# Performance work log

Measured on AMD Instinct MI355X. Metric: run time of the kernel, lower is better.

## Reference

```python
import jax, jax.numpy as jnp
import numpy as np

B, H, W, C = 8, 64, 64, 64


def setup_inputs() -> dict:
    key = jax.random.key(0)
    ks = jax.random.split(key, 9)
    s = 1.0 / np.sqrt(C)
    return {
        "x": jax.random.normal(ks[0], (B, H, W, C), dtype=jnp.float32),
        "wq": jax.random.uniform(ks[1], (C, C), jnp.float32, -s, s),
        "bq": jax.random.uniform(ks[2], (C,), jnp.float32, -s, s),
        "wk": jax.random.uniform(ks[3], (C, C), jnp.float32, -s, s),
        "bk": jax.random.uniform(ks[4], (C,), jnp.float32, -s, s),
        "wv": jax.random.uniform(ks[5], (C, C), jnp.float32, -s, s),
        "bv": jax.random.uniform(ks[6], (C,), jnp.float32, -s, s),
        "wp": jax.random.uniform(ks[7], (C, C), jnp.float32, -s, s),
        "bp": jax.random.uniform(ks[8], (C,), jnp.float32, -s, s),
    }


def reference(x, wq, bq, wk, bk, wv, bv, wp, bp):
    b, h, w, c = x.shape
    n = h * w
    xf = x.reshape(b, n, c)
    scale = c ** (-0.5)
    q = xf @ wq.T + bq  # [B,N,C]
    k = xf @ wk.T + bk
    v = xf @ wv.T + bv
    center_idx = (h // 2) * w + (w // 2)
    central = q[:, center_idx, :][:, None, :]           # [B,1,C]
    qb = jnp.broadcast_to(central, (b, n, c))           # rank-1 broadcast query
    pos = jnp.arange(n)
    dist = jnp.sqrt(((pos // w - h // 2) ** 2 + (pos % w - w // 2) ** 2).astype(jnp.float32))
    weights = jnp.exp(1.0 - dist)                       # [N]
    qw = qb * weights[None, :, None]
    attn = jnp.einsum('bnc,bmc->bnm', qw, k) * scale    # dense [B,N,N] (memory-bound)
    attn = jax.nn.softmax(attn, axis=-1)
    out = jnp.einsum('bnm,bmc->bnc', attn, v)
    out = out @ wp.T + bp
    return out.reshape(b, h, w, c)
```

## Files before the change

### kernel.cpp

```cpp
#include <hip/hip_runtime.h>

#define BB 8
#define NN 4096
#define CC 64
#define CENTER (32*64 + 32)
#define GTILE 16
#define MS 32
#define MSL (NN/MS)
#define CUT 64

struct Geom {
    short gid[2049];
    short g2d2[64];
    int ng;
};

constexpr Geom makeGeom() {
    Geom t{};
    bool occ[2049] = {};
    for (int y = 0; y < 64; ++y)
        for (int x = 0; x < 64; ++x) {
            int dy = y - 32, dx = x - 32;
            occ[dy*dy + dx*dx] = true;
        }
    int g = 0;
    for (int i = 0; i < CUT; ++i) {
        if (occ[i]) { t.gid[i] = (short)g; t.g2d2[g] = (short)i; ++g; }
        else t.gid[i] = (short)-1;
    }
    t.ng = g;
    for (int i = CUT; i <= 2048; ++i) t.gid[i] = occ[i] ? (short)g : (short)-1;
    return t;
}

constexpr int NGN = makeGeom().ng;
constexpr int NT  = (NGN + 1 + GTILE - 1) / GTILE;
constexpr int GE  = NT * GTILE;
static_assert(NGN + 1 <= GE, "group padding");
static_assert(MS * 8 == 256, "blockIdx decode shift");
__constant__ Geom GEOM = makeGeom();

constexpr int CST_WVPT = 0;
constexpr int CST_BVP  = 4096;
constexpr int CST_U    = 4160;
constexpr int CST_T    = 4672;
constexpr int CST_SIZE = 4736;

constexpr int OFF_CST  = 0;
constexpr int OFF_S    = CST_SIZE;
constexpr int OFF_VP   = OFF_S + BB*NN;
constexpr int OFF_PART = OFF_VP + BB*NN*CC;
constexpr int OFF_ZP   = OFF_PART + BB*MS*GE*CC;
constexpr int OFF_OG   = OFF_ZP + BB*MS*GE;

__global__ __launch_bounds__(256) void k_prep(
    const float* __restrict__ x,
    const float* __restrict__ wq, const float* __restrict__ bq,
    const float* __restrict__ wk, const float* __restrict__ bk,
    const float* __restrict__ wv, const float* __restrict__ bv,
    const float* __restrict__ wp,
    float* __restrict__ cst)
{
    const int tid = threadIdx.x;
    const int blk = blockIdx.x;
    if (blk < 8) {
        __shared__ float q_s[CC];
        const int b = blk;
        if (tid < CC) {
            const float* xc = x + ((size_t)b*NN + CENTER)*CC;
            float a = bq[tid];
            for (int i = 0; i < CC; ++i) a += xc[i] * wq[tid*CC + i];
            q_s[tid] = a;
        }
        __syncthreads();
        if (tid < CC) {
            float a = 0.f;
            for (int c = 0; c < CC; ++c) a += q_s[c] * wk[c*CC + tid];
            cst[CST_U + b*CC + tid] = a;
        }
        if (tid == 64) {
            float a = 0.f;
            for (int c = 0; c < CC; ++c) a += q_s[c] * bk[c];
            cst[CST_T + b] = a;
        }
    } else if (blk < 24) {
        const int idx = (blk - 8)*256 + tid;
        const int i = idx >> 6, c = idx & 63;
        float a = 0.f;
        for (int j = 0; j < CC; ++j) a += wp[c*CC + j] * wv[j*CC + i];
        cst[CST_WVPT + idx] = a;
    } else {
        if (tid < CC) {
            float a = 0.f;
            for (int j = 0; j < CC; ++j) a += wp[tid*CC + j] * bv[j];
            cst[CST_BVP + tid] = a;
        }
    }
}

__global__ __launch_bounds__(256) void k_vps(
    const float* __restrict__ x, const float* __restrict__ cst,
    float* __restrict__ s_out, float* __restrict__ vp_out)
{
    const int tid = threadIdx.x;
    const int cq  = blockIdx.x & 3;
    const int row = (blockIdx.x >> 2)*256 + tid;
    const int b   = blockIdx.x >> 6;

    float4 xr[16];
    const float4* x4 = (const float4*)(x + (size_t)row * CC);
    #pragma unroll
    for (int i = 0; i < 16; ++i) xr[i] = x4[i];

    if (cq == 0) {
        const float* u = cst + CST_U + b*CC;
        float sa = cst[CST_T + b];
        #pragma unroll
        for (int i4 = 0; i4 < 16; ++i4) {
            sa += xr[i4].x*u[i4*4+0] + xr[i4].y*u[i4*4+1]
                + xr[i4].z*u[i4*4+2] + xr[i4].w*u[i4*4+3];
        }
        s_out[row] = sa * 0.125f;
    }

    const int c0 = cq * 16;
    float4 acc[4];
    #pragma unroll
    for (int k = 0; k < 4; ++k) {
        acc[k].x = cst[CST_BVP + c0 + k*4 + 0];
        acc[k].y = cst[CST_BVP + c0 + k*4 + 1];
        acc[k].z = cst[CST_BVP + c0 + k*4 + 2];
        acc[k].w = cst[CST_BVP + c0 + k*4 + 3];
    }
    #pragma unroll
    for (int i = 0; i < 64; ++i) {
        const float xv = ((const float*)xr)[i];
        const float* wr = cst + CST_WVPT + i*CC + c0;
        #pragma unroll
        for (int k = 0; k < 4; ++k) {
            acc[k].x += xv * wr[k*4+0];
            acc[k].y += xv * wr[k*4+1];
            acc[k].z += xv * wr[k*4+2];
            acc[k].w += xv * wr[k*4+3];
        }
    }
    float4* vp4 = (float4*)vp_out + (size_t)row*16 + cq*4;
    #pragma unroll
    for (int k = 0; k < 4; ++k) vp4[k] = acc[k];
}

#define FMA4(A, E, V) do { (A).x += (E)*(V).x; (A).y += (E)*(V).y; \
                           (A).z += (E)*(V).z; (A).w += (E)*(V).w; } while(0)

__global__ __launch_bounds__(256) void k_attn(
    const float* __restrict__ sA, const float* __restrict__ vpA,
    float* __restrict__ part, float* __restrict__ zpart)
{
    __shared__ __align__(16) float Es[MSL*GTILE];
    __shared__ __align__(16) float red[4*GTILE*GTILE*4];
    __shared__ float zred[4*GTILE];
    __shared__ float w_s[GTILE];

    const int tid = threadIdx.x;
    const int b   = blockIdx.x & 7;
    const int ms  = (blockIdx.x >> 3) & (MS - 1);
    const int gt  = blockIdx.x >> 8;
    const int g0  = gt * GTILE;
    const int m0  = ms * MSL;

    if (tid < GTILE) {
        const int g = g0 + tid;
        w_s[tid] = (g < NGN) ? __expf(1.f - sqrtf((float)GEOM.g2d2[g])) : 0.f;
    }
    __syncthreads();

    const int gE = tid & 15;
    const int mE = tid >> 4;
    const float wg = w_s[gE];
    const int c4 = tid & 15;

    float zacc = 0.f;
    float4 acc[GTILE];
    #pragma unroll
    for (int g = 0; g < GTILE; ++g) acc[g] = make_float4(0.f, 0.f, 0.f, 0.f);

    const float* s_row = sA + b*NN + m0;
    const float4* vp4  = (const float4*)vpA + ((size_t)b*NN + m0)*16;
    const float4* E4   = (const float4*)Es;

    #pragma unroll
    for (int p = 0; p < MSL/16; ++p) {
        const int ml = mE + 16*p;
        const float e = __expf(wg * s_row[ml]);
        Es[ml*GTILE + gE] = e;
        zacc += e;
    }
    __syncthreads();
    #pragma unroll
    for (int p = 0; p < MSL/16; ++p) {
        const int ml = mE + 16*p;
        const float4 v4 = vp4[(size_t)ml*16 + c4];
        float4 e4;
        e4 = E4[ml*4 + 0];
        FMA4(acc[0],  e4.x, v4); FMA4(acc[1],  e4.y, v4);
        FMA4(acc[2],  e4.z, v4); FMA4(acc[3],  e4.w, v4);
        e4 = E4[ml*4 + 1];
        FMA4(acc[4],  e4.x, v4); FMA4(acc[5],  e4.y, v4);
        FMA4(acc[6],  e4.z, v4); FMA4(acc[7],  e4.w, v4);
        e4 = E4[ml*4 + 2];
        FMA4(acc[8],  e4.x, v4); FMA4(acc[9],  e4.y, v4);
        FMA4(acc[10], e4.z, v4); FMA4(acc[11], e4.w, v4);
        e4 = E4[ml*4 + 3];
        FMA4(acc[12], e4.x, v4); FMA4(acc[13], e4.y, v4);
        FMA4(acc[14], e4.z, v4); FMA4(acc[15], e4.w, v4);
    }
    __syncthreads();

    const int l  = tid & 63;
    const int wv = tid >> 6;
    #pragma unroll
    for (int g = 0; g < GTILE; ++g) {
        acc[g].x += __shfl_xor(acc[g].x, 16, 64);
        acc[g].y += __shfl_xor(acc[g].y, 16, 64);
        acc[g].z += __shfl_xor(acc[g].z, 16, 64);
        acc[g].w += __shfl_xor(acc[g].w, 16, 64);
        acc[g].x += __shfl_xor(acc[g].x, 32, 64);
        acc[g].y += __shfl_xor(acc[g].y, 32, 64);
        acc[g].z += __shfl_xor(acc[g].z, 32, 64);
        acc[g].w += __shfl_xor(acc[g].w, 32, 64);
    }
    zacc += __shfl_xor(zacc, 16, 64);
    zacc += __shfl_xor(zacc, 32, 64);

    float4* red4 = (float4*)red;
    if (l < 16) {
        #pragma unroll
        for (int g = 0; g < GTILE; ++g)
            red4[(wv*GTILE + g)*GTILE + l] = acc[g];
        zred[wv*16 + l] = zacc;
    }
    __syncthreads();

    {
        const int g = tid >> 4, c = tid & 15;
        float4 o0 = red4[(0*GTILE + g)*GTILE + c];
        float4 o1 = red4[(1*GTILE + g)*GTILE + c];
        float4 o2 = red4[(2*GTILE + g)*GTILE + c];
        float4 o3 = red4[(3*GTILE + g)*GTILE + c];
        o0.x += o1.x + o2.x + o3.x;
        o0.y += o1.y + o2.y + o3.y;
        o0.z += o1.z + o2.z + o3.z;
        o0.w += o1.w + o2.w + o3.w;
        ((float4*)part)[(size_t)((b*MS + ms)*GE + g0 + g)*16 + c] = o0;
        if (tid < 16) {
            float Zg = zred[tid] + zred[16+tid] + zred[32+tid] + zred[48+tid];
            zpart[(b*MS + ms)*GE + g0 + tid] = Zg;
        }
    }
}

__global__ __launch_bounds__(256) void k_red(
    const float* __restrict__ part, const float* __restrict__ zpart,
    const float* __restrict__ bp, float* __restrict__ og)
{
    const int idx = blockIdx.x*256 + threadIdx.x;
    const int bg  = idx >> 6;
    const int b   = bg / GE, g = bg - b*GE;
    const int c   = idx & 63;
    float a = 0.f, z = 0.f;
    #pragma unroll 8
    for (int ms = 0; ms < MS; ++ms) {
        a += part[(size_t)((b*MS + ms)*GE + g)*CC + c];
        z += zpart[(b*MS + ms)*GE + g];
    }
    og[(size_t)bg*CC + c] = a / z + bp[c];
}

__global__ __launch_bounds__(256) void k_out(
    const float* __restrict__ og, float* __restrict__ out)
{
    const int i4 = blockIdx.x * 256 + threadIdx.x;
    const int c4 = i4 & 15;
    const int n  = (i4 >> 4) & (NN - 1);
    const int b  = i4 >> 16;
    const int dy = (n >> 6) - 32, dx = (n & 63) - 32;
    const int g  = GEOM.gid[dy*dy + dx*dx];
    ((float4*)out)[i4] = ((const float4*)og)[(size_t)(b*GE + g)*16 + c4];
}

extern "C" void kernel_launch(void* const* d_in, const int* in_sizes, int n_in,
                              void* d_out, int out_size, void* d_ws, size_t ws_size,
                              hipStream_t stream) {
    const float* x  = (const float*)d_in[0];
    const float* wq = (const float*)d_in[1];
    const float* bq = (const float*)d_in[2];
    const float* wk = (const float*)d_in[3];
    const float* bk = (const float*)d_in[4];
    const float* wv = (const float*)d_in[5];
    const float* bv = (const float*)d_in[6];
    const float* wp = (const float*)d_in[7];
    const float* bp = (const float*)d_in[8];
    float* ws = (float*)d_ws;

    k_prep<<<25, 256, 0, stream>>>(x, wq, bq, wk, bk, wv, bv, wp, ws + OFF_CST);
    k_vps<<<512, 256, 0, stream>>>(x, ws + OFF_CST, ws + OFF_S, ws + OFF_VP);
    k_attn<<<NT*MS*8, 256, 0, stream>>>(ws + OFF_S, ws + OFF_VP,
                                        ws + OFF_PART, ws + OFF_ZP);
    k_red<<<(BB*GE*CC)/256, 256, 0, stream>>>(ws + OFF_PART, ws + OFF_ZP,
                                              bp, ws + OFF_OG);
    k_out<<<2048, 256, 0, stream>>>(ws + OFF_OG, (float*)d_out);
}
```

Measured before the change: 104.3 us.

## Fuse value projection and scores into attention kernel, keep vp in LDS

Merges the k_vps projection kernel into the attention kernel. Each block computes the projected values and scores for its 64-row slice directly into shared memory, so the large vp intermediate no longer goes to global memory and one launch is removed. All group tiles (GE=32) are handled in a single block by looping over two halves, and MS rises to 64 to keep the grid at 512 blocks. In exchange, each block recomputes the projection with per-thread accumulators and uses more LDS, which may lower occupancy, and there are twice as many partials to reduce.

Measured after the change: 119.3 us. +14.3%, slower.

```diff
diff --git a/kernel.cpp b/kernel.cpp
--- a/kernel.cpp
+++ b/kernel.cpp
@@ -4,8 +4,7 @@
 #define NN 4096
 #define CC 64
 #define CENTER (32*64 + 32)
-#define GTILE 16
-#define MS 32
+#define MS 64
 #define MSL (NN/MS)
 #define CUT 64
 
@@ -34,10 +33,8 @@
 }
 
 constexpr int NGN = makeGeom().ng;
-constexpr int NT  = (NGN + 1 + GTILE - 1) / GTILE;
-constexpr int GE  = NT * GTILE;
+constexpr int GE  = 32;
 static_assert(NGN + 1 <= GE, "group padding");
-static_assert(MS * 8 == 256, "blockIdx decode shift");
 __constant__ Geom GEOM = makeGeom();
 
 constexpr int CST_WVPT = 0;
@@ -47,9 +44,7 @@
 constexpr int CST_SIZE = 4736;
 
 constexpr int OFF_CST  = 0;
-constexpr int OFF_S    = CST_SIZE;
-constexpr int OFF_VP   = OFF_S + BB*NN;
-constexpr int OFF_PART = OFF_VP + BB*NN*CC;
+constexpr int OFF_PART = CST_SIZE;
 constexpr int OFF_ZP   = OFF_PART + BB*MS*GE*CC;
 constexpr int OFF_OG   = OFF_ZP + BB*MS*GE;
 
@@ -98,164 +93,130 @@
     }
 }
 
-__global__ __launch_bounds__(256) void k_vps(
-    const float* __restrict__ x, const float* __restrict__ cst,
-    float* __restrict__ s_out, float* __restrict__ vp_out)
-{
-    const int tid = threadIdx.x;
-    const int cq  = blockIdx.x & 3;
-    const int row = (blockIdx.x >> 2)*256 + tid;
-    const int b   = blockIdx.x >> 6;
-
-    float4 xr[16];
-    const float4* x4 = (const float4*)(x + (size_t)row * CC);
-    #pragma unroll
-    for (int i = 0; i < 16; ++i) xr[i] = x4[i];
-
-    if (cq == 0) {
-        const float* u = cst + CST_U + b*CC;
-        float sa = cst[CST_T + b];
-        #pragma unroll
-        for (int i4 = 0; i4 < 16; ++i4) {
-            sa += xr[i4].x*u[i4*4+0] + xr[i4].y*u[i4*4+1]
-                + xr[i4].z*u[i4*4+2] + xr[i4].w*u[i4*4+3];
-        }
-        s_out[row] = sa * 0.125f;
-    }
-
-    const int c0 = cq * 16;
-    float4 acc[4];
-    #pragma unroll
-    for (int k = 0; k < 4; ++k) {
-        acc[k].x = cst[CST_BVP + c0 + k*4 + 0];
-        acc[k].y = cst[CST_BVP + c0 + k*4 + 1];
-        acc[k].z = cst[CST_BVP + c0 + k*4 + 2];
-        acc[k].w = cst[CST_BVP + c0 + k*4 + 3];
-    }
-    #pragma unroll
-    for (int i = 0; i < 64; ++i) {
-        const float xv = ((const float*)xr)[i];
-        const float* wr = cst + CST_WVPT + i*CC + c0;
-        #pragma unroll
-        for (int k = 0; k < 4; ++k) {
-            acc[k].x += xv * wr[k*4+0];
-            acc[k].y += xv * wr[k*4+1];
-            acc[k].z += xv * wr[k*4+2];
-            acc[k].w += xv * wr[k*4+3];
-        }
-    }
-    float4* vp4 = (float4*)vp_out + (size_t)row*16 + cq*4;
-    #pragma unroll
-    for (int k = 0; k < 4; ++k) vp4[k] = acc[k];
-}
-
 #define FMA4(A, E, V) do { (A).x += (E)*(V).x; (A).y += (E)*(V).y; \
                            (A).z += (E)*(V).z; (A).w += (E)*(V).w; } while(0)
 
-__global__ __launch_bounds__(256) void k_attn(
-    const float* __restrict__ sA, const float* __restrict__ vpA,
+__global__ __launch_bounds__(256) void k_main(
+    const float* __restrict__ x, const float* __restrict__ cst,
     float* __restrict__ part, float* __restrict__ zpart)
 {
-    __shared__ __align__(16) float Es[MSL*GTILE];
-    __shared__ __align__(16) float red[4*GTILE*GTILE*4];
-    __shared__ float zred[4*GTILE];
-    __shared__ float w_s[GTILE];
+    __shared__ __align__(16) float vp_s[MSL*68];
+    __shared__ __align__(16) float Es[MSL*36];
+    __shared__ float s_s[MSL];
+    __shared__ __align__(16) float4 red4[4*16*16];
+    __shared__ float zred[4*GE];
 
     const int tid = threadIdx.x;
     const int b   = blockIdx.x & 7;
-    const int ms  = (blockIdx.x >> 3) & (MS - 1);
-    const int gt  = blockIdx.x >> 8;
-    const int g0  = gt * GTILE;
+    const int ms  = blockIdx.x >> 3;
     const int m0  = ms * MSL;
-
-    if (tid < GTILE) {
-        const int g = g0 + tid;
-        w_s[tid] = (g < NGN) ? __expf(1.f - sqrtf((float)GEOM.g2d2[g])) : 0.f;
-    }
+    const int w   = tid >> 6;
+    const int l   = tid & 63;
+
+    const int c0 = __builtin_amdgcn_readfirstlane(w * 16);
+    const int row = m0 + l;
+    const float4* xrow4 = (const float4*)(x + ((size_t)b*NN + row)*CC);
+    const float* wvpT = cst + CST_WVPT;
+    const float* u    = cst + CST_U + b*CC;
+
+    float acc1[16];
+    #pragma unroll
+    for (int k = 0; k < 16; ++k) acc1[k] = cst[CST_BVP + c0 + k];
+    float sa = cst[CST_T + b];
+
+    #pragma unroll
+    for (int i4 = 0; i4 < 16; ++i4) {
+        const float4 xi = xrow4[i4];
+        if (w == 0)
+            sa += xi.x*u[i4*4+0] + xi.y*u[i4*4+1] + xi.z*u[i4*4+2] + xi.w*u[i4*4+3];
+        const float xv[4] = {xi.x, xi.y, xi.z, xi.w};
+        #pragma unroll
+        for (int ii = 0; ii < 4; ++ii) {
+            const float* wr = wvpT + (i4*4 + ii)*CC + c0;
+            #pragma unroll
+            for (int k = 0; k < 16; ++k) acc1[k] += xv[ii] * wr[k];
+        }
+    }
+    if (w == 0) s_s[l] = sa * 0.125f;
+    #pragma unroll
+    for (int k4 = 0; k4 < 4; ++k4)
+        *(float4*)&vp_s[l*68 + c0 + k4*4] =
+            make_float4(acc1[k4*4+0], acc1[k4*4+1], acc1[k4*4+2], acc1[k4*4+3]);
     __syncthreads();
 
-    const int gE = tid & 15;
+    const int gE = tid & 31;
+    const float wg = (gE < NGN) ? __expf(1.f - sqrtf((float)GEOM.g2d2[gE])) : 0.f;
+    const int mh = tid >> 5;
+    float zacc = 0.f;
+    #pragma unroll
+    for (int p = 0; p < 8; ++p) {
+        const int m = mh + 8*p;
+        const float e = __expf(wg * s_s[m]);
+        Es[m*36 + gE] = e;
+        zacc += e;
+    }
+    zacc += __shfl_xor(zacc, 32, 64);
+    if (l < 32) zred[w*32 + l] = zacc;
+    __syncthreads();
+
+    const int c4 = tid & 15;
     const int mE = tid >> 4;
-    const float wg = w_s[gE];
-    const int c4 = tid & 15;
-
-    float zacc = 0.f;
-    float4 acc[GTILE];
-    #pragma unroll
-    for (int g = 0; g < GTILE; ++g) acc[g] = make_float4(0.f, 0.f, 0.f, 0.f);
-
-    const float* s_row = sA + b*NN + m0;
-    const float4* vp4  = (const float4*)vpA + ((size_t)b*NN + m0)*16;
-    const float4* E4   = (const float4*)Es;
-
-    #pragma unroll
-    for (int p = 0; p < MSL/16; ++p) {
-        const int ml = mE + 16*p;
-        const float e = __expf(wg * s_row[ml]);
-        Es[ml*GTILE + gE] = e;
-        zacc += e;
-    }
-    __syncthreads();
-    #pragma unroll
-    for (int p = 0; p < MSL/16; ++p) {
-        const int ml = mE + 16*p;
-        const float4 v4 = vp4[(size_t)ml*16 + c4];
-        float4 e4;
-        e4 = E4[ml*4 + 0];
-        FMA4(acc[0],  e4.x, v4); FMA4(acc[1],  e4.y, v4);
-        FMA4(acc[2],  e4.z, v4); FMA4(acc[3],  e4.w, v4);
-        e4 = E4[ml*4 + 1];
-        FMA4(acc[4],  e4.x, v4); FMA4(acc[5],  e4.y, v4);
-        FMA4(acc[6],  e4.z, v4); FMA4(acc[7],  e4.w, v4);
-        e4 = E4[ml*4 + 2];
-        FMA4(acc[8],  e4.x, v4); FMA4(acc[9],  e4.y, v4);
-        FMA4(acc[10], e4.z, v4); FMA4(acc[11], e4.w, v4);
-        e4 = E4[ml*4 + 3];
-        FMA4(acc[12], e4.x, v4); FMA4(acc[13], e4.y, v4);
-        FMA4(acc[14], e4.z, v4); FMA4(acc[15], e4.w, v4);
-    }
-    __syncthreads();
-
-    const int l  = tid & 63;
-    const int wv = tid >> 6;
-    #pragma unroll
-    for (int g = 0; g < GTILE; ++g) {
-        acc[g].x += __shfl_xor(acc[g].x, 16, 64);
-        acc[g].y += __shfl_xor(acc[g].y, 16, 64);
-        acc[g].z += __shfl_xor(acc[g].z, 16, 64);
-        acc[g].w += __shfl_xor(acc[g].w, 16, 64);
-        acc[g].x += __shfl_xor(acc[g].x, 32, 64);
-        acc[g].y += __shfl_xor(acc[g].y, 32, 64);
-        acc[g].z += __shfl_xor(acc[g].z, 32, 64);
-        acc[g].w += __shfl_xor(acc[g].w, 32, 64);
-    }
-    zacc += __shfl_xor(zacc, 16, 64);
-    zacc += __shfl_xor(zacc, 32, 64);
-
-    float4* red4 = (float4*)red;
-    if (l < 16) {
-        #pragma unroll
-        for (int g = 0; g < GTILE; ++g)
-            red4[(wv*GTILE + g)*GTILE + l] = acc[g];
-        zred[wv*16 + l] = zacc;
-    }
-    __syncthreads();
-
-    {
-        const int g = tid >> 4, c = tid & 15;
-        float4 o0 = red4[(0*GTILE + g)*GTILE + c];
-        float4 o1 = red4[(1*GTILE + g)*GTILE + c];
-        float4 o2 = red4[(2*GTILE + g)*GTILE + c];
-        float4 o3 = red4[(3*GTILE + g)*GTILE + c];
-        o0.x += o1.x + o2.x + o3.x;
-        o0.y += o1.y + o2.y + o3.y;
-        o0.z += o1.z + o2.z + o3.z;
-        o0.w += o1.w + o2.w + o3.w;
-        ((float4*)part)[(size_t)((b*MS + ms)*GE + g0 + g)*16 + c] = o0;
-        if (tid < 16) {
-            float Zg = zred[tid] + zred[16+tid] + zred[32+tid] + zred[48+tid];
-            zpart[(b*MS + ms)*GE + g0 + tid] = Zg;
-        }
+    for (int gh = 0; gh < 2; ++gh) {
+        float4 acc[16];
+        #pragma unroll
+        for (int g = 0; g < 16; ++g) acc[g] = make_float4(0.f, 0.f, 0.f, 0.f);
+        #pragma unroll
+        for (int p = 0; p < 4; ++p) {
+            const int m = mE + 16*p;
+            const float4 v4 = *(const float4*)&vp_s[m*68 + c4*4];
+            const float4 e0 = *(const float4*)&Es[m*36 + gh*16 + 0];
+            const float4 e1 = *(const float4*)&Es[m*36 + gh*16 + 4];
+            const float4 e2 = *(const float4*)&Es[m*36 + gh*16 + 8];
+            const float4 e3 = *(const float4*)&Es[m*36 + gh*16 + 12];
+            FMA4(acc[0],  e0.x, v4); FMA4(acc[1],  e0.y, v4);
+            FMA4(acc[2],  e0.z, v4); FMA4(acc[3],  e0.w, v4);
+            FMA4(acc[4],  e1.x, v4); FMA4(acc[5],  e1.y, v4);
+            FMA4(acc[6],  e1.z, v4); FMA4(acc[7],  e1.w, v4);
+            FMA4(acc[8],  e2.x, v4); FMA4(acc[9],  e2.y, v4);
+            FMA4(acc[10], e2.z, v4); FMA4(acc[11], e2.w, v4);
+            FMA4(acc[12], e3.x, v4); FMA4(acc[13], e3.y, v4);
+            FMA4(acc[14], e3.z, v4); FMA4(acc[15], e3.w, v4);
+        }
+        #pragma unroll
+        for (int g = 0; g < 16; ++g) {
+            acc[g].x += __shfl_xor(acc[g].x, 16, 64);
+            acc[g].y += __shfl_xor(acc[g].y, 16, 64);
+            acc[g].z += __shfl_xor(acc[g].z, 16, 64);
+            acc[g].w += __shfl_xor(acc[g].w, 16, 64);
+            acc[g].x += __shfl_xor(acc[g].x, 32, 64);
+            acc[g].y += __shfl_xor(acc[g].y, 32, 64);
+            acc[g].z += __shfl_xor(acc[g].z, 32, 64);
+            acc[g].w += __shfl_xor(acc[g].w, 32, 64);
+        }
+        if (l < 16) {
+            #pragma unroll
+            for (int g = 0; g < 16; ++g)
+                red4[(w*16 + g)*16 + l] = acc[g];
+        }
+        __syncthreads();
+        {
+            const int g = tid >> 4, c = tid & 15;
+            float4 o0 = red4[(0*16 + g)*16 + c];
+            float4 o1 = red4[(1*16 + g)*16 + c];
+            float4 o2 = red4[(2*16 + g)*16 + c];
+            float4 o3 = red4[(3*16 + g)*16 + c];
+            o0.x += o1.x + o2.x + o3.x;
+            o0.y += o1.y + o2.y + o3.y;
+            o0.z += o1.z + o2.z + o3.z;
+            o0.w += o1.w + o2.w + o3.w;
+            ((float4*)part)[(size_t)((b*MS + ms)*GE + gh*16 + g)*16 + c] = o0;
+        }
+        __syncthreads();
+    }
+
+    if (tid < GE) {
+        float Z = zred[tid] + zred[GE + tid] + zred[2*GE + tid] + zred[3*GE + tid];
+        zpart[(b*MS + ms)*GE + tid] = Z;
     }
 }
 
@@ -265,7 +226,7 @@
 {
     const int idx = blockIdx.x*256 + threadIdx.x;
     const int bg  = idx >> 6;
-    const int b   = bg / GE, g = bg - b*GE;
+    const int b   = bg >> 5, g = bg & 31;
     const int c   = idx & 63;
     float a = 0.f, z = 0.f;
     #pragma unroll 8
@@ -303,9 +264,7 @@
     float* ws = (float*)d_ws;
 
     k_prep<<<25, 256, 0, stream>>>(x, wq, bq, wk, bk, wv, bv, wp, ws + OFF_CST);
-    k_vps<<<512, 256, 0, stream>>>(x, ws + OFF_CST, ws + OFF_S, ws + OFF_VP);
-    k_attn<<<NT*MS*8, 256, 0, stream>>>(ws + OFF_S, ws + OFF_VP,
-                                        ws + OFF_PART, ws + OFF_ZP);
+    k_main<<<MS*8, 256, 0, stream>>>(x, ws + OFF_CST, ws + OFF_PART, ws + OFF_ZP);
     k_red<<<(BB*GE*CC)/256, 256, 0, stream>>>(ws + OFF_PART, ws + OFF_ZP,
                                               bp, ws + OFF_OG);
     k_out<<<2048, 256, 0, stream>>>(ws + OFF_OG, (float*)d_out);
```
